# Kernel optimization log

Hardware: AMD Instinct MI355X
Metric: run time of the kernel (lower is better)

Reference implementation:

```python
import jax, jax.numpy as jnp
import numpy as np

REGION = (4, 4, 4)
NHEAD = 4
HEAD_DIM = 64
SCALE = HEAD_DIM ** -0.5
NUM_MODALITIES = 4


def _grid2seq(x, region, nhead):
    # x: [B, C, H, W, D] -> [B, nhead, n_regions, region_cube, head_dim]
    B, C, H, W, D = x.shape
    rh, rw, rd = H // region[0], W // region[1], D // region[2]
    hd = C // nhead
    x = x.reshape(B, nhead, hd, rh, region[0], rw, region[1], rd, region[2])
    x = x.transpose(0, 1, 3, 5, 7, 4, 6, 8, 2)  # bmchpwqdr -> bmhwdpqrc
    return x.reshape(B, nhead, rh * rw * rd, region[0] * region[1] * region[2], hd), rh, rw, rd


def _seq2grid(x, rh, rw, rd, region):
    # x: [B, nhead, n_regions, region_cube, head_dim] -> [B, C, H, W, D]
    B, nhead, nreg, rc, hd = x.shape
    x = x.reshape(B, nhead, rh, rw, rd, region[0], region[1], region[2], hd)
    x = x.transpose(0, 1, 8, 2, 5, 3, 6, 4, 7)  # bmhwdpqrc -> bmchpwqdr
    return x.reshape(B, nhead * hd, rh * region[0], rw * region[1], rd * region[2])


def _gather_regions(kv_seq, rg):
    # kv_seq: [B, H, kvN, kc, hd], rg: [B, H, qN, topk] -> [B, H, qN, topk, kc, hd]
    return jax.vmap(jax.vmap(lambda k, g: k[g]))(kv_seq, rg)


def setup_inputs() -> dict:
    key = jax.random.key(0)
    ks = jax.random.split(key, 20)
    shp = (2, 256, 16, 16, 16)
    inp = {"mask": jnp.ones((2, 4), dtype=jnp.int32)}
    names = [f"{p}{i}" for p in ("q", "k", "v") for i in range(4)]
    for n, kk in zip(names, ks[:12]):
        inp[n] = jax.random.normal(kk, shp, dtype=jnp.float32)
    for i, kk in zip(range(4), ks[12:16]):
        inp[f"rg{i}"] = jax.random.randint(kk, (2, 4, 64, 4), 0, 64, dtype=jnp.int32)
    return inp


def reference(mask, q0, q1, q2, q3, k0, k1, k2, k3, v0, v1, v2, v3, rg0, rg1, rg2, rg3):
    qs = [q0, q1, q2, q3]
    ks = [k0, k1, k2, k3]
    vs = [v0, v1, v2, v3]
    rgs = [rg0, rg1, rg2, rg3]

    q_seq, rh, rw, rd = zip(*[(g[0], g[1], g[2], g[3]) for g in [_grid2seq(q, REGION, NHEAD) for q in qs]])
    rh, rw, rd = rh[0], rw[0], rd[0]

    key_parts, val_parts = [], []
    for k_, v_, rg_ in zip(ks, vs, rgs):
        kseq, _, _, _ = _grid2seq(k_, REGION, NHEAD)
        vseq, _, _, _ = _grid2seq(v_, REGION, NHEAD)
        B, H, kvN, kc, hd = kseq.shape
        qN = rg_.shape[2]
        kg = _gather_regions(kseq, rg_).reshape(B, H, qN, -1, hd)  # [B,H,qN,topk*kc,hd]
        vg = _gather_regions(vseq, rg_).reshape(B, H, qN, -1, hd)
        key_parts.append(kg)
        val_parts.append(vg)
    key_g = jnp.concatenate(key_parts, axis=-2)  # [B,H,qN, M*topk*kc, hd]
    value_g = jnp.concatenate(val_parts, axis=-2)

    N = key_g.shape[-2]
    rep = N // NUM_MODALITIES
    mask_full = jnp.repeat(mask[:, None, None, None, :], rep, axis=-1)  # [B,1,1,1,N]

    outs = []
    for q in q_seq:
        attn = jnp.einsum("bhnqc,bhnkc->bhnqk", q * SCALE, key_g)
        attn = jnp.where(mask_full == 0, -jnp.inf, attn)
        attn = jax.nn.softmax(attn, axis=-1)
        o = jnp.einsum("bhnqk,bhnkc->bhnqc", attn, value_g)
        outs.append(_seq2grid(o, rh, rw, rd, REGION))
    return jnp.stack(outs, axis=0)  # [M, B, C, H, W, D]
```

## Files before the change

kernel.cpp:

```cpp
#include <hip/hip_runtime.h>
#include <hip/hip_bf16.h>

typedef short v8s __attribute__((ext_vector_type(8)));
typedef float v4f __attribute__((ext_vector_type(4)));

#define LDK 72
#define SCALE_LOG2E 0.18033688f
#define RESCALE_THR 8.0f

struct MMRAParams {
    const float* q[4];
    const float* k[4];
    const float* v[4];
    const int*   rg[4];
    const int*   mask;
    float*       out;
};

__device__ __forceinline__ unsigned pkbf(float a, float b) {
    unsigned r;
    asm("v_cvt_pk_bf16_f32 %0, %1, %2" : "=v"(r) : "v"(a), "v"(b));
    return r;
}

__global__ __launch_bounds__(256, 2)
void mmra_attn(MMRAParams P) {
    const int bid = blockIdx.x;
    const int h = bid & 3;
    const int b = (bid >> 2) & 1;
    const int n = bid >> 3;
    const int H0 = ((n >> 4) & 3) << 2;
    const int W0 = ((n >> 2) & 3) << 2;
    const int D0 = (n & 3) << 2;

    const int tid  = threadIdx.x;
    const int wave = tid >> 6;
    const int lane = tid & 63;
    const int l15  = lane & 15;
    const int quad = lane >> 4;

    __shared__ __align__(16) ushort Klds[64 * LDK];
    __shared__ __align__(16) ushort Vlds[64 * LDK];
    __shared__ __align__(16) ushort Plds[4][64 * LDK];

    const int bh_base = (b * 256 + h * 64) * 4096;
    const int rgbase  = ((b * 4 + h) * 64 + n) * 4;

    const bool actm[4] = { P.mask[b * 4 + 0] != 0, P.mask[b * 4 + 1] != 0,
                           P.mask[b * 4 + 2] != 0, P.mask[b * 4 + 3] != 0 };

    auto kptr = [&](int m) { return (m == 0) ? P.k[0] : (m == 1) ? P.k[1] : (m == 2) ? P.k[2] : P.k[3]; };
    auto vptr = [&](int m) { return (m == 0) ? P.v[0] : (m == 1) ? P.v[1] : (m == 2) ? P.v[2] : P.v[3]; };
    auto rptr = [&](int m) { return (m == 0) ? P.rg[0] : (m == 1) ? P.rg[1] : (m == 2) ? P.rg[2] : P.rg[3]; };

    float4 pkf[4], pvf[4];
    auto prefetch = [&](int cj) {
        const int mod = cj >> 2, j = cj & 3;
        const int g = rptr(mod)[rgbase + j] & 63;
        const int goff = (((g >> 4) & 3) << 10) + (((g >> 2) & 3) << 6) + ((g & 3) << 2);
        const float* ks = kptr(mod);
        const float* vs = vptr(mod);
        const int off0 = bh_base + lane * 4096 + goff;
        #pragma unroll
        for (int i = 0; i < 4; ++i) {
            const int pq = wave * 4 + i;
            const int off = off0 + (pq >> 2) * 256 + (pq & 3) * 16;
            pkf[i] = *(const float4*)(ks + off);
            pvf[i] = *(const float4*)(vs + off);
        }
    };

    prefetch(0);

    v8s qfrag[4][2];
    {
        ushort* qbuf = &Plds[wave][0];
        const float* qsrc = (wave == 0) ? P.q[0] : (wave == 1) ? P.q[1] : (wave == 2) ? P.q[2] : P.q[3];
        #pragma unroll
        for (int rb = 0; rb < 4; ++rb) {
            #pragma unroll
            for (int i = 0; i < 4; ++i) {
                int off = bh_base + lane * 4096 + (H0 + rb) * 256 + (W0 + i) * 16 + D0;
                float4 cv = *(const float4*)(qsrc + off);
                unsigned q01 = pkbf(cv.x * SCALE_LOG2E, cv.y * SCALE_LOG2E);
                unsigned q23 = pkbf(cv.z * SCALE_LOG2E, cv.w * SCALE_LOG2E);
                ushort* qb = &qbuf[(rb * 16 + i * 4) * LDK + lane];
                qb[0 * LDK] = (ushort)q01;
                qb[1 * LDK] = (ushort)(q01 >> 16);
                qb[2 * LDK] = (ushort)q23;
                qb[3 * LDK] = (ushort)(q23 >> 16);
            }
        }
        __asm__ volatile("s_waitcnt lgkmcnt(0)" ::: "memory");
        #pragma unroll
        for (int rb = 0; rb < 4; ++rb) {
            qfrag[rb][0] = *(const v8s*)&qbuf[(rb * 16 + l15) * LDK + quad * 8];
            qfrag[rb][1] = *(const v8s*)&qbuf[(rb * 16 + l15) * LDK + 32 + quad * 8];
        }
    }

    v4f  oacc[4][4];
    float mrow[4], lrow[4];
    #pragma unroll
    for (int mt = 0; mt < 4; ++mt) {
        mrow[mt] = -1e30f; lrow[mt] = 0.f;
        #pragma unroll
        for (int nt = 0; nt < 4; ++nt) oacc[mt][nt] = (v4f){0.f, 0.f, 0.f, 0.f};
    }

    #pragma unroll 1
    for (int cj = 0; cj < 16; ++cj) {
        const bool act = actm[cj >> 2];
        if (act) {
            __syncthreads();
            #pragma unroll
            for (int i = 0; i < 4; ++i) {
                const int pq = wave * 4 + i;
                unsigned k01 = pkbf(pkf[i].x, pkf[i].y);
                unsigned k23 = pkbf(pkf[i].z, pkf[i].w);
                ushort* kb = &Klds[(pq * 4) * LDK + lane];
                kb[0 * LDK] = (ushort)k01;
                kb[1 * LDK] = (ushort)(k01 >> 16);
                kb[2 * LDK] = (ushort)k23;
                kb[3 * LDK] = (ushort)(k23 >> 16);
                uint2 vv;
                vv.x = pkbf(pvf[i].x, pvf[i].y);
                vv.y = pkbf(pvf[i].z, pvf[i].w);
                *(uint2*)&Vlds[lane * LDK + pq * 4] = vv;
            }
        }
        if (cj < 15) prefetch(cj + 1);
        if (!act) continue;
        __syncthreads();

        {
            v8s kfrag[4][2];
            #pragma unroll
            for (int t = 0; t < 4; ++t) {
                kfrag[t][0] = *(const v8s*)&Klds[(t * 16 + l15) * LDK + quad * 8];
                kfrag[t][1] = *(const v8s*)&Klds[(t * 16 + l15) * LDK + 32 + quad * 8];
            }
            #pragma unroll
            for (int mt = 0; mt < 4; ++mt) {
                float sv[4][4];
                #pragma unroll
                for (int nt = 0; nt < 4; ++nt) {
                    v4f acc = (v4f){0.f, 0.f, 0.f, 0.f};
                    acc = __builtin_amdgcn_mfma_f32_16x16x32_bf16(kfrag[nt][0], qfrag[mt][0], acc, 0, 0, 0);
                    acc = __builtin_amdgcn_mfma_f32_16x16x32_bf16(kfrag[nt][1], qfrag[mt][1], acc, 0, 0, 0);
                    #pragma unroll
                    for (int r = 0; r < 4; ++r) sv[nt][r] = acc[r];
                }
                float mx;
                {
                    float a0 = fmaxf(fmaxf(sv[0][0], sv[0][1]), sv[0][2]);
                    float a1 = fmaxf(fmaxf(sv[0][3], sv[1][0]), sv[1][1]);
                    float a2 = fmaxf(fmaxf(sv[1][2], sv[1][3]), sv[2][0]);
                    float a3 = fmaxf(fmaxf(sv[2][1], sv[2][2]), sv[2][3]);
                    float a4 = fmaxf(fmaxf(sv[3][0], sv[3][1]), sv[3][2]);
                    mx = fmaxf(fmaxf(fmaxf(a0, a1), a2), fmaxf(fmaxf(a3, a4), sv[3][3]));
                }
                mx = fmaxf(mx, __shfl_xor(mx, 16));
                mx = fmaxf(mx, __shfl_xor(mx, 32));

                if (!__all(mx - mrow[mt] <= RESCALE_THR)) {
                    const float mnew  = fmaxf(mrow[mt], mx);
                    const float alpha = exp2f(mrow[mt] - mnew);
                    mrow[mt] = mnew;
                    lrow[mt] *= alpha;
                    float alpha_row[4];
                    #pragma unroll
                    for (int r = 0; r < 4; ++r)
                        alpha_row[r] = __shfl(alpha, (quad << 4) | (quad * 4 + r));
                    #pragma unroll
                    for (int nt = 0; nt < 4; ++nt)
                        #pragma unroll
                        for (int r = 0; r < 4; ++r) oacc[mt][nt][r] *= alpha_row[r];
                }
                const float mcur = mrow[mt];

                float rsum = 0.f;
                #pragma unroll
                for (int nt = 0; nt < 4; ++nt) {
                    float p0 = exp2f(sv[nt][0] - mcur);
                    float p1 = exp2f(sv[nt][1] - mcur);
                    float p2 = exp2f(sv[nt][2] - mcur);
                    float p3 = exp2f(sv[nt][3] - mcur);
                    rsum += (p0 + p1) + (p2 + p3);
                    uint2 pw;
                    pw.x = pkbf(p0, p1);
                    pw.y = pkbf(p2, p3);
                    *(uint2*)&Plds[wave][(mt * 16 + l15) * LDK + nt * 16 + quad * 4] = pw;
                }
                rsum += __shfl_xor(rsum, 16);
                rsum += __shfl_xor(rsum, 32);
                lrow[mt] += rsum;
            }
        }

        __asm__ volatile("s_waitcnt lgkmcnt(0)" ::: "memory");
        {
            v8s vfrag[4][2];
            #pragma unroll
            for (int t = 0; t < 4; ++t) {
                vfrag[t][0] = *(const v8s*)&Vlds[(t * 16 + l15) * LDK + quad * 8];
                vfrag[t][1] = *(const v8s*)&Vlds[(t * 16 + l15) * LDK + 32 + quad * 8];
            }
            #pragma unroll
            for (int mt = 0; mt < 4; ++mt) {
                v8s pf0 = *(const v8s*)&Plds[wave][(mt * 16 + l15) * LDK + quad * 8];
                v8s pf1 = *(const v8s*)&Plds[wave][(mt * 16 + l15) * LDK + 32 + quad * 8];
                #pragma unroll
                for (int nt = 0; nt < 4; ++nt) {
                    oacc[mt][nt] = __builtin_amdgcn_mfma_f32_16x16x32_bf16(pf0, vfrag[nt][0], oacc[mt][nt], 0, 0, 0);
                    oacc[mt][nt] = __builtin_amdgcn_mfma_f32_16x16x32_bf16(pf1, vfrag[nt][1], oacc[mt][nt], 0, 0, 0);
                }
            }
        }
    }

    const int obase = (wave * 2 + b) * 1048576 + h * 64 * 4096;
    #pragma unroll
    for (int mt = 0; mt < 4; ++mt) {
        const float invq = 1.0f / lrow[mt];
        float inv_row[4];
        #pragma unroll
        for (int r = 0; r < 4; ++r)
            inv_row[r] = __shfl(invq, (quad << 4) | (quad * 4 + r));
        #pragma unroll
        for (int nt = 0; nt < 4; ++nt) {
            float4 ov;
            ov.x = oacc[mt][nt][0] * inv_row[0];
            ov.y = oacc[mt][nt][1] * inv_row[1];
            ov.z = oacc[mt][nt][2] * inv_row[2];
            ov.w = oacc[mt][nt][3] * inv_row[3];
            int off = obase + (nt * 16 + l15) * 4096 + (H0 + mt) * 256 + (W0 + quad) * 16 + D0;
            *(float4*)(P.out + off) = ov;
        }
    }
}

extern "C" void kernel_launch(void* const* d_in, const int* in_sizes, int n_in,
                              void* d_out, int out_size, void* d_ws, size_t ws_size,
                              hipStream_t stream) {
    (void)in_sizes; (void)n_in; (void)out_size; (void)d_ws; (void)ws_size;
    MMRAParams P;
    P.mask = (const int*)d_in[0];
    for (int i = 0; i < 4; ++i) {
        P.q[i]  = (const float*)d_in[1 + i];
        P.k[i]  = (const float*)d_in[5 + i];
        P.v[i]  = (const float*)d_in[9 + i];
        P.rg[i] = (const int*)d_in[13 + i];
    }
    P.out = (float*)d_out;
    hipLaunchKernelGGL(mmra_attn, dim3(512), dim3(256), 0, stream, P);
}
```

Before: 238.5 us.

## Split query rows across 8 waves and keep P in registers for PV

Doubles the block to 512 threads so each of the 8 waves handles half of one modality's query rows. K and V staging work per wave is halved. The P matrix is no longer written to and read back from LDS: its register layout is fed directly into 16x16x16 bf16 MFMAs against transposed V fragments, removing the per-wave P buffers and a wait on LDS. It relies on the accumulator layout matching the MFMA A-operand layout, and it doubles the MFMA instruction count for PV because each instruction covers half the K depth.

```diff
diff --git a/kernel.cpp b/kernel.cpp
--- a/kernel.cpp
+++ b/kernel.cpp
@@ -2,6 +2,7 @@
 #include <hip/hip_bf16.h>
 
 typedef short v8s __attribute__((ext_vector_type(8)));
+typedef short v4s __attribute__((ext_vector_type(4)));
 typedef float v4f __attribute__((ext_vector_type(4)));
 
 #define LDK 72
@@ -23,7 +24,18 @@
     return r;
 }
 
-__global__ __launch_bounds__(256, 2)
+__device__ __forceinline__ v4f mfma16(v4s a, v4s b, v4f c) {
+#if __has_builtin(__builtin_amdgcn_mfma_f32_16x16x16bf16_1k)
+    return __builtin_amdgcn_mfma_f32_16x16x16bf16_1k(a, b, c, 0, 0, 0);
+#elif __has_builtin(__builtin_amdgcn_mfma_f32_16x16x16_bf16)
+    return __builtin_amdgcn_mfma_f32_16x16x16_bf16(a, b, c, 0, 0, 0);
+#else
+    asm("v_mfma_f32_16x16x16_bf16 %0, %1, %2, %0" : "+v"(c) : "v"(a), "v"(b));
+    return c;
+#endif
+}
+
+__global__ __launch_bounds__(512, 4)
 void mmra_attn(MMRAParams P) {
     const int bid = blockIdx.x;
     const int h = bid & 3;
@@ -35,13 +47,15 @@
 
     const int tid  = threadIdx.x;
     const int wave = tid >> 6;
+    const int qm   = wave >> 1;
+    const int mth  = wave & 1;
     const int lane = tid & 63;
     const int l15  = lane & 15;
     const int quad = lane >> 4;
 
-    __shared__ __align__(16) ushort Klds[64 * LDK];
-    __shared__ __align__(16) ushort Vlds[64 * LDK];
-    __shared__ __align__(16) ushort Plds[4][64 * LDK];
+    __shared__ __align__(16) ushort SMEM[18432];
+    ushort* Klds = SMEM;
+    ushort* Vlds = SMEM + 4608;
 
     const int bh_base = (b * 256 + h * 64) * 4096;
     const int rgbase  = ((b * 4 + h) * 64 + n) * 4;
@@ -53,7 +67,7 @@
     auto vptr = [&](int m) { return (m == 0) ? P.v[0] : (m == 1) ? P.v[1] : (m == 2) ? P.v[2] : P.v[3]; };
     auto rptr = [&](int m) { return (m == 0) ? P.rg[0] : (m == 1) ? P.rg[1] : (m == 2) ? P.rg[2] : P.rg[3]; };
 
-    float4 pkf[4], pvf[4];
+    float4 pkf[2], pvf[2];
     auto prefetch = [&](int cj) {
         const int mod = cj >> 2, j = cj & 3;
         const int g = rptr(mod)[rgbase + j] & 63;
@@ -62,8 +76,8 @@
         const float* vs = vptr(mod);
         const int off0 = bh_base + lane * 4096 + goff;
         #pragma unroll
-        for (int i = 0; i < 4; ++i) {
-            const int pq = wave * 4 + i;
+        for (int i = 0; i < 2; ++i) {
+            const int pq = wave * 2 + i;
             const int off = off0 + (pq >> 2) * 256 + (pq & 3) * 16;
             pkf[i] = *(const float4*)(ks + off);
             pvf[i] = *(const float4*)(vs + off);
@@ -72,19 +86,20 @@
 
     prefetch(0);
 
-    v8s qfrag[4][2];
+    v8s qfrag[2][2];
     {
-        ushort* qbuf = &Plds[wave][0];
-        const float* qsrc = (wave == 0) ? P.q[0] : (wave == 1) ? P.q[1] : (wave == 2) ? P.q[2] : P.q[3];
-        #pragma unroll
-        for (int rb = 0; rb < 4; ++rb) {
+        ushort* qbuf = SMEM + wave * 2304;
+        const float* qsrc = (qm == 0) ? P.q[0] : (qm == 1) ? P.q[1] : (qm == 2) ? P.q[2] : P.q[3];
+        #pragma unroll
+        for (int rb2 = 0; rb2 < 2; ++rb2) {
+            const int rb = mth * 2 + rb2;
             #pragma unroll
             for (int i = 0; i < 4; ++i) {
                 int off = bh_base + lane * 4096 + (H0 + rb) * 256 + (W0 + i) * 16 + D0;
                 float4 cv = *(const float4*)(qsrc + off);
                 unsigned q01 = pkbf(cv.x * SCALE_LOG2E, cv.y * SCALE_LOG2E);
                 unsigned q23 = pkbf(cv.z * SCALE_LOG2E, cv.w * SCALE_LOG2E);
-                ushort* qb = &qbuf[(rb * 16 + i * 4) * LDK + lane];
+                ushort* qb = &qbuf[(rb2 * 16 + i * 4) * LDK + lane];
                 qb[0 * LDK] = (ushort)q01;
                 qb[1 * LDK] = (ushort)(q01 >> 16);
                 qb[2 * LDK] = (ushort)q23;
@@ -93,19 +108,19 @@
         }
         __asm__ volatile("s_waitcnt lgkmcnt(0)" ::: "memory");
         #pragma unroll
-        for (int rb = 0; rb < 4; ++rb) {
-            qfrag[rb][0] = *(const v8s*)&qbuf[(rb * 16 + l15) * LDK + quad * 8];
-            qfrag[rb][1] = *(const v8s*)&qbuf[(rb * 16 + l15) * LDK + 32 + quad * 8];
-        }
-    }
-
-    v4f  oacc[4][4];
-    float mrow[4], lrow[4];
+        for (int m2 = 0; m2 < 2; ++m2) {
+            qfrag[m2][0] = *(const v8s*)&qbuf[(m2 * 16 + l15) * LDK + quad * 8];
+            qfrag[m2][1] = *(const v8s*)&qbuf[(m2 * 16 + l15) * LDK + 32 + quad * 8];
+        }
+    }
+
+    v4f  oacc[2][4];
+    float mrow[2], lrow[2];
     #pragma unroll
-    for (int mt = 0; mt < 4; ++mt) {
-        mrow[mt] = -1e30f; lrow[mt] = 0.f;
-        #pragma unroll
-        for (int nt = 0; nt < 4; ++nt) oacc[mt][nt] = (v4f){0.f, 0.f, 0.f, 0.f};
+    for (int m2 = 0; m2 < 2; ++m2) {
+        mrow[m2] = -1e30f; lrow[m2] = 0.f;
+        #pragma unroll
+        for (int t = 0; t < 4; ++t) oacc[m2][t] = (v4f){0.f, 0.f, 0.f, 0.f};
     }
 
     #pragma unroll 1
@@ -114,8 +129,8 @@
         if (act) {
             __syncthreads();
             #pragma unroll
-            for (int i = 0; i < 4; ++i) {
-                const int pq = wave * 4 + i;
+            for (int i = 0; i < 2; ++i) {
+                const int pq = wave * 2 + i;
                 unsigned k01 = pkbf(pkf[i].x, pkf[i].y);
                 unsigned k23 = pkbf(pkf[i].z, pkf[i].w);
                 ushort* kb = &Klds[(pq * 4) * LDK + lane];
@@ -133,108 +148,97 @@
         if (!act) continue;
         __syncthreads();
 
+        uint2 pa[2][4];
         {
-            v8s kfrag[4][2];
-            #pragma unroll
-            for (int t = 0; t < 4; ++t) {
-                kfrag[t][0] = *(const v8s*)&Klds[(t * 16 + l15) * LDK + quad * 8];
-                kfrag[t][1] = *(const v8s*)&Klds[(t * 16 + l15) * LDK + 32 + quad * 8];
-            }
-            #pragma unroll
-            for (int mt = 0; mt < 4; ++mt) {
-                float sv[4][4];
+            float sv[2][4][4];
+            #pragma unroll
+            for (int nt = 0; nt < 4; ++nt) {
+                v8s kf0 = *(const v8s*)&Klds[(nt * 16 + l15) * LDK + quad * 8];
+                v8s kf1 = *(const v8s*)&Klds[(nt * 16 + l15) * LDK + 32 + quad * 8];
                 #pragma unroll
-                for (int nt = 0; nt < 4; ++nt) {
+                for (int m2 = 0; m2 < 2; ++m2) {
                     v4f acc = (v4f){0.f, 0.f, 0.f, 0.f};
-                    acc = __builtin_amdgcn_mfma_f32_16x16x32_bf16(kfrag[nt][0], qfrag[mt][0], acc, 0, 0, 0);
-                    acc = __builtin_amdgcn_mfma_f32_16x16x32_bf16(kfrag[nt][1], qfrag[mt][1], acc, 0, 0, 0);
+                    acc = __builtin_amdgcn_mfma_f32_16x16x32_bf16(kf0, qfrag[m2][0], acc, 0, 0, 0);
+                    acc = __builtin_amdgcn_mfma_f32_16x16x32_bf16(kf1, qfrag[m2][1], acc, 0, 0, 0);
                     #pragma unroll
-                    for (int r = 0; r < 4; ++r) sv[nt][r] = acc[r];
-                }
+                    for (int r = 0; r < 4; ++r) sv[m2][nt][r] = acc[r];
+                }
+            }
+            #pragma unroll
+            for (int m2 = 0; m2 < 2; ++m2) {
                 float mx;
                 {
-                    float a0 = fmaxf(fmaxf(sv[0][0], sv[0][1]), sv[0][2]);
-                    float a1 = fmaxf(fmaxf(sv[0][3], sv[1][0]), sv[1][1]);
-                    float a2 = fmaxf(fmaxf(sv[1][2], sv[1][3]), sv[2][0]);
-                    float a3 = fmaxf(fmaxf(sv[2][1], sv[2][2]), sv[2][3]);
-                    float a4 = fmaxf(fmaxf(sv[3][0], sv[3][1]), sv[3][2]);
-                    mx = fmaxf(fmaxf(fmaxf(a0, a1), a2), fmaxf(fmaxf(a3, a4), sv[3][3]));
+                    float a0 = fmaxf(fmaxf(sv[m2][0][0], sv[m2][0][1]), sv[m2][0][2]);
+                    float a1 = fmaxf(fmaxf(sv[m2][0][3], sv[m2][1][0]), sv[m2][1][1]);
+                    float a2 = fmaxf(fmaxf(sv[m2][1][2], sv[m2][1][3]), sv[m2][2][0]);
+                    float a3 = fmaxf(fmaxf(sv[m2][2][1], sv[m2][2][2]), sv[m2][2][3]);
+                    float a4 = fmaxf(fmaxf(sv[m2][3][0], sv[m2][3][1]), sv[m2][3][2]);
+                    mx = fmaxf(fmaxf(fmaxf(a0, a1), a2), fmaxf(fmaxf(a3, a4), sv[m2][3][3]));
                 }
                 mx = fmaxf(mx, __shfl_xor(mx, 16));
                 mx = fmaxf(mx, __shfl_xor(mx, 32));
 
-                if (!__all(mx - mrow[mt] <= RESCALE_THR)) {
-                    const float mnew  = fmaxf(mrow[mt], mx);
-                    const float alpha = exp2f(mrow[mt] - mnew);
-                    mrow[mt] = mnew;
-                    lrow[mt] *= alpha;
+                if (!__all(mx - mrow[m2] <= RESCALE_THR)) {
+                    const float mnew  = fmaxf(mrow[m2], mx);
+                    const float alpha = exp2f(mrow[m2] - mnew);
+                    mrow[m2] = mnew;
+                    lrow[m2] *= alpha;
                     float alpha_row[4];
                     #pragma unroll
                     for (int r = 0; r < 4; ++r)
                         alpha_row[r] = __shfl(alpha, (quad << 4) | (quad * 4 + r));
                     #pragma unroll
-                    for (int nt = 0; nt < 4; ++nt)
+                    for (int t = 0; t < 4; ++t)
                         #pragma unroll
-                        for (int r = 0; r < 4; ++r) oacc[mt][nt][r] *= alpha_row[r];
-                }
-                const float mcur = mrow[mt];
+                        for (int r = 0; r < 4; ++r) oacc[m2][t][r] *= alpha_row[r];
+                }
+                const float mcur = mrow[m2];
 
                 float rsum = 0.f;
                 #pragma unroll
                 for (int nt = 0; nt < 4; ++nt) {
-                    float p0 = exp2f(sv[nt][0] - mcur);
-                    float p1 = exp2f(sv[nt][1] - mcur);
-                    float p2 = exp2f(sv[nt][2] - mcur);
-                    float p3 = exp2f(sv[nt][3] - mcur);
+                    float p0 = exp2f(sv[m2][nt][0] - mcur);
+                    float p1 = exp2f(sv[m2][nt][1] - mcur);
+                    float p2 = exp2f(sv[m2][nt][2] - mcur);
+                    float p3 = exp2f(sv[m2][nt][3] - mcur);
                     rsum += (p0 + p1) + (p2 + p3);
-                    uint2 pw;
-                    pw.x = pkbf(p0, p1);
-                    pw.y = pkbf(p2, p3);
-                    *(uint2*)&Plds[wave][(mt * 16 + l15) * LDK + nt * 16 + quad * 4] = pw;
+                    pa[m2][nt].x = pkbf(p0, p1);
+                    pa[m2][nt].y = pkbf(p2, p3);
                 }
                 rsum += __shfl_xor(rsum, 16);
                 rsum += __shfl_xor(rsum, 32);
-                lrow[mt] += rsum;
-            }
-        }
-
-        __asm__ volatile("s_waitcnt lgkmcnt(0)" ::: "memory");
-        {
-            v8s vfrag[4][2];
-            #pragma unroll
-            for (int t = 0; t < 4; ++t) {
-                vfrag[t][0] = *(const v8s*)&Vlds[(t * 16 + l15) * LDK + quad * 8];
-                vfrag[t][1] = *(const v8s*)&Vlds[(t * 16 + l15) * LDK + 32 + quad * 8];
-            }
-            #pragma unroll
-            for (int mt = 0; mt < 4; ++mt) {
-                v8s pf0 = *(const v8s*)&Plds[wave][(mt * 16 + l15) * LDK + quad * 8];
-                v8s pf1 = *(const v8s*)&Plds[wave][(mt * 16 + l15) * LDK + 32 + quad * 8];
-                #pragma unroll
-                for (int nt = 0; nt < 4; ++nt) {
-                    oacc[mt][nt] = __builtin_amdgcn_mfma_f32_16x16x32_bf16(pf0, vfrag[nt][0], oacc[mt][nt], 0, 0, 0);
-                    oacc[mt][nt] = __builtin_amdgcn_mfma_f32_16x16x32_bf16(pf1, vfrag[nt][1], oacc[mt][nt], 0, 0, 0);
-                }
-            }
-        }
-    }
-
-    const int obase = (wave * 2 + b) * 1048576 + h * 64 * 4096;
+                lrow[m2] += rsum;
+            }
+        }
+
+        #pragma unroll
+        for (int t = 0; t < 4; ++t) {
+            #pragma unroll
+            for (int nt = 0; nt < 4; ++nt) {
+                v4s vf = *(const v4s*)&Vlds[(t * 16 + l15) * LDK + nt * 16 + quad * 4];
+                oacc[0][t] = mfma16(__builtin_bit_cast(v4s, pa[0][nt]), vf, oacc[0][t]);
+                oacc[1][t] = mfma16(__builtin_bit_cast(v4s, pa[1][nt]), vf, oacc[1][t]);
+            }
+        }
+    }
+
+    const int obase = (qm * 2 + b) * 1048576 + h * 64 * 4096;
     #pragma unroll
-    for (int mt = 0; mt < 4; ++mt) {
-        const float invq = 1.0f / lrow[mt];
+    for (int m2 = 0; m2 < 2; ++m2) {
+        const int mt = mth * 2 + m2;
+        const float invq = 1.0f / lrow[m2];
         float inv_row[4];
         #pragma unroll
         for (int r = 0; r < 4; ++r)
             inv_row[r] = __shfl(invq, (quad << 4) | (quad * 4 + r));
         #pragma unroll
-        for (int nt = 0; nt < 4; ++nt) {
+        for (int t = 0; t < 4; ++t) {
             float4 ov;
-            ov.x = oacc[mt][nt][0] * inv_row[0];
-            ov.y = oacc[mt][nt][1] * inv_row[1];
-            ov.z = oacc[mt][nt][2] * inv_row[2];
-            ov.w = oacc[mt][nt][3] * inv_row[3];
-            int off = obase + (nt * 16 + l15) * 4096 + (H0 + mt) * 256 + (W0 + quad) * 16 + D0;
+            ov.x = oacc[m2][t][0] * inv_row[0];
+            ov.y = oacc[m2][t][1] * inv_row[1];
+            ov.z = oacc[m2][t][2] * inv_row[2];
+            ov.w = oacc[m2][t][3] * inv_row[3];
+            int off = obase + (t * 16 + l15) * 4096 + (H0 + mt) * 256 + (W0 + quad) * 16 + D0;
             *(float4*)(P.out + off) = ov;
         }
     }
@@ -253,5 +257,5 @@
         P.rg[i] = (const int*)d_in[13 + i];
     }
     P.out = (float*)d_out;
-    hipLaunchKernelGGL(mmra_attn, dim3(512), dim3(256), 0, stream, P);
-}
+    hipLaunchKernelGGL(mmra_attn, dim3(512), dim3(512), 0, stream, P);
+}
```

Measured after the change: 240.4 us. Within noise of the previous version (+0.8%).

## Double-buffer K/V in LDS and keep P in registers for PV MFMA

Applied to the files above, without the earlier changes.

Replaces the single K/V LDS buffer with a double buffer, so the next chunk is staged while the current one is computed, and drops one barrier per iteration. It precomputes a list of active modality chunks so masked chunks are skipped without per-iteration branching. The softmax probabilities stay in registers and feed 16x16x16 bf16 MFMAs directly instead of going through a per-wave P buffer in LDS. It also adds s_setprio around the MFMA blocks. The cost is more live registers (the full score tile plus packed P), which could reduce occupancy or cause spills, and twice as many smaller MFMAs in the PV product.

```diff
diff --git a/kernel.cpp b/kernel.cpp
--- a/kernel.cpp
+++ b/kernel.cpp
@@ -2,6 +2,7 @@
 #include <hip/hip_bf16.h>
 
 typedef short v8s __attribute__((ext_vector_type(8)));
+typedef short v4s __attribute__((ext_vector_type(4)));
 typedef float v4f __attribute__((ext_vector_type(4)));
 
 #define LDK 72
@@ -21,6 +22,17 @@
     unsigned r;
     asm("v_cvt_pk_bf16_f32 %0, %1, %2" : "=v"(r) : "v"(a), "v"(b));
     return r;
+}
+
+__device__ __forceinline__ v4f mfma16(v4s a, v4s b, v4f c) {
+#if __has_builtin(__builtin_amdgcn_mfma_f32_16x16x16bf16_1k)
+    return __builtin_amdgcn_mfma_f32_16x16x16bf16_1k(a, b, c, 0, 0, 0);
+#elif __has_builtin(__builtin_amdgcn_mfma_f32_16x16x16_bf16)
+    return __builtin_amdgcn_mfma_f32_16x16x16_bf16(a, b, c, 0, 0, 0);
+#else
+    asm("v_mfma_f32_16x16x16_bf16 %0, %1, %2, %0" : "+v"(c) : "v"(a), "v"(b));
+    return c;
+#endif
 }
 
 __global__ __launch_bounds__(256, 2)
@@ -39,9 +51,7 @@
     const int l15  = lane & 15;
     const int quad = lane >> 4;
 
-    __shared__ __align__(16) ushort Klds[64 * LDK];
-    __shared__ __align__(16) ushort Vlds[64 * LDK];
-    __shared__ __align__(16) ushort Plds[4][64 * LDK];
+    __shared__ __align__(16) ushort SMEM[18432];
 
     const int bh_base = (b * 256 + h * 64) * 4096;
     const int rgbase  = ((b * 4 + h) * 64 + n) * 4;
@@ -52,6 +62,14 @@
     auto kptr = [&](int m) { return (m == 0) ? P.k[0] : (m == 1) ? P.k[1] : (m == 2) ? P.k[2] : P.k[3]; };
     auto vptr = [&](int m) { return (m == 0) ? P.v[0] : (m == 1) ? P.v[1] : (m == 2) ? P.v[2] : P.v[3]; };
     auto rptr = [&](int m) { return (m == 0) ? P.rg[0] : (m == 1) ? P.rg[1] : (m == 2) ? P.rg[2] : P.rg[3]; };
+
+    unsigned long long clist = 0ull; int nc = 0;
+    for (int m = 0; m < 4; ++m) {
+        if (actm[m]) {
+            #pragma unroll
+            for (int s = 0; s < 4; ++s) { clist |= ((unsigned long long)(m * 4 + s)) << (4 * nc); ++nc; }
+        }
+    }
 
     float4 pkf[4], pvf[4];
     auto prefetch = [&](int cj) {
@@ -70,11 +88,31 @@
         }
     };
 
-    prefetch(0);
+    auto stage = [&](int buf) {
+        ushort* Kb = SMEM + buf * 9216;
+        ushort* Vb = Kb + 4608;
+        #pragma unroll
+        for (int i = 0; i < 4; ++i) {
+            const int pq = wave * 4 + i;
+            unsigned k01 = pkbf(pkf[i].x, pkf[i].y);
+            unsigned k23 = pkbf(pkf[i].z, pkf[i].w);
+            ushort* kb = &Kb[(pq * 4) * LDK + lane];
+            kb[0 * LDK] = (ushort)k01;
+            kb[1 * LDK] = (ushort)(k01 >> 16);
+            kb[2 * LDK] = (ushort)k23;
+            kb[3 * LDK] = (ushort)(k23 >> 16);
+            uint2 vv;
+            vv.x = pkbf(pvf[i].x, pvf[i].y);
+            vv.y = pkbf(pvf[i].z, pvf[i].w);
+            *(uint2*)&Vb[lane * LDK + pq * 4] = vv;
+        }
+    };
+
+    prefetch((int)(clist & 15));
 
     v8s qfrag[4][2];
     {
-        ushort* qbuf = &Plds[wave][0];
+        ushort* qbuf = SMEM + wave * 4608;
         const float* qsrc = (wave == 0) ? P.q[0] : (wave == 1) ? P.q[1] : (wave == 2) ? P.q[2] : P.q[3];
         #pragma unroll
         for (int rb = 0; rb < 4; ++rb) {
@@ -98,6 +136,10 @@
             qfrag[rb][1] = *(const v8s*)&qbuf[(rb * 16 + l15) * LDK + 32 + quad * 8];
         }
     }
+    __syncthreads();
+    stage(0);
+    if (nc > 1) prefetch((int)((clist >> 4) & 15));
+    __syncthreads();
 
     v4f  oacc[4][4];
     float mrow[4], lrow[4];
@@ -105,118 +147,97 @@
     for (int mt = 0; mt < 4; ++mt) {
         mrow[mt] = -1e30f; lrow[mt] = 0.f;
         #pragma unroll
-        for (int nt = 0; nt < 4; ++nt) oacc[mt][nt] = (v4f){0.f, 0.f, 0.f, 0.f};
-    }
-
+        for (int t = 0; t < 4; ++t) oacc[mt][t] = (v4f){0.f, 0.f, 0.f, 0.f};
+    }
+
+    int cur = 0;
     #pragma unroll 1
-    for (int cj = 0; cj < 16; ++cj) {
-        const bool act = actm[cj >> 2];
-        if (act) {
-            __syncthreads();
-            #pragma unroll
-            for (int i = 0; i < 4; ++i) {
-                const int pq = wave * 4 + i;
-                unsigned k01 = pkbf(pkf[i].x, pkf[i].y);
-                unsigned k23 = pkbf(pkf[i].z, pkf[i].w);
-                ushort* kb = &Klds[(pq * 4) * LDK + lane];
-                kb[0 * LDK] = (ushort)k01;
-                kb[1 * LDK] = (ushort)(k01 >> 16);
-                kb[2 * LDK] = (ushort)k23;
-                kb[3 * LDK] = (ushort)(k23 >> 16);
-                uint2 vv;
-                vv.x = pkbf(pvf[i].x, pvf[i].y);
-                vv.y = pkbf(pvf[i].z, pvf[i].w);
-                *(uint2*)&Vlds[lane * LDK + pq * 4] = vv;
-            }
-        }
-        if (cj < 15) prefetch(cj + 1);
-        if (!act) continue;
+    for (int i = 0; i < nc; ++i) {
+        if (i + 1 < nc) {
+            stage(cur ^ 1);
+            if (i + 2 < nc) prefetch((int)((clist >> (4 * (i + 2))) & 15));
+        }
+        const ushort* Kb = SMEM + cur * 9216;
+        const ushort* Vb = Kb + 4608;
+
+        float sv[4][4][4];
+        #pragma unroll
+        for (int nt = 0; nt < 4; ++nt) {
+            v8s kf0 = *(const v8s*)&Kb[(nt * 16 + l15) * LDK + quad * 8];
+            v8s kf1 = *(const v8s*)&Kb[(nt * 16 + l15) * LDK + 32 + quad * 8];
+            __builtin_amdgcn_s_setprio(1);
+            #pragma unroll
+            for (int mt = 0; mt < 4; ++mt) {
+                v4f acc = (v4f){0.f, 0.f, 0.f, 0.f};
+                acc = __builtin_amdgcn_mfma_f32_16x16x32_bf16(kf0, qfrag[mt][0], acc, 0, 0, 0);
+                acc = __builtin_amdgcn_mfma_f32_16x16x32_bf16(kf1, qfrag[mt][1], acc, 0, 0, 0);
+                #pragma unroll
+                for (int r = 0; r < 4; ++r) sv[mt][nt][r] = acc[r];
+            }
+            __builtin_amdgcn_s_setprio(0);
+        }
+        uint2 pa[4][4];
+        #pragma unroll
+        for (int mt = 0; mt < 4; ++mt) {
+            float mx;
+            {
+                float a0 = fmaxf(fmaxf(sv[mt][0][0], sv[mt][0][1]), sv[mt][0][2]);
+                float a1 = fmaxf(fmaxf(sv[mt][0][3], sv[mt][1][0]), sv[mt][1][1]);
+                float a2 = fmaxf(fmaxf(sv[mt][1][2], sv[mt][1][3]), sv[mt][2][0]);
+                float a3 = fmaxf(fmaxf(sv[mt][2][1], sv[mt][2][2]), sv[mt][2][3]);
+                float a4 = fmaxf(fmaxf(sv[mt][3][0], sv[mt][3][1]), sv[mt][3][2]);
+                mx = fmaxf(fmaxf(fmaxf(a0, a1), a2), fmaxf(fmaxf(a3, a4), sv[mt][3][3]));
+            }
+            mx = fmaxf(mx, __shfl_xor(mx, 16));
+            mx = fmaxf(mx, __shfl_xor(mx, 32));
+
+            if (!__all(mx - mrow[mt] <= RESCALE_THR)) {
+                const float mnew  = fmaxf(mrow[mt], mx);
+                const float alpha = exp2f(mrow[mt] - mnew);
+                mrow[mt] = mnew;
+                lrow[mt] *= alpha;
+                float alpha_row[4];
+                #pragma unroll
+                for (int r = 0; r < 4; ++r)
+                    alpha_row[r] = __shfl(alpha, (quad << 4) | (quad * 4 + r));
+                #pragma unroll
+                for (int t = 0; t < 4; ++t)
+                    #pragma unroll
+                    for (int r = 0; r < 4; ++r) oacc[mt][t][r] *= alpha_row[r];
+            }
+            const float mcur = mrow[mt];
+
+            float rsum = 0.f;
+            #pragma unroll
+            for (int nt = 0; nt < 4; ++nt) {
+                float p0 = exp2f(sv[mt][nt][0] - mcur);
+                float p1 = exp2f(sv[mt][nt][1] - mcur);
+                float p2 = exp2f(sv[mt][nt][2] - mcur);
+                float p3 = exp2f(sv[mt][nt][3] - mcur);
+                rsum += (p0 + p1) + (p2 + p3);
+                pa[mt][nt].x = pkbf(p0, p1);
+                pa[mt][nt].y = pkbf(p2, p3);
+            }
+            rsum += __shfl_xor(rsum, 16);
+            rsum += __shfl_xor(rsum, 32);
+            lrow[mt] += rsum;
+        }
+
+        __builtin_amdgcn_s_setprio(1);
+        #pragma unroll
+        for (int t = 0; t < 4; ++t) {
+            #pragma unroll
+            for (int nt = 0; nt < 4; ++nt) {
+                v4s vf = *(const v4s*)&Vb[(t * 16 + l15) * LDK + nt * 16 + quad * 4];
+                #pragma unroll
+                for (int mt = 0; mt < 4; ++mt)
+                    oacc[mt][t] = mfma16(__builtin_bit_cast(v4s, pa[mt][nt]), vf, oacc[mt][t]);
+            }
+        }
+        __builtin_amdgcn_s_setprio(0);
+
         __syncthreads();
-
-        {
-            v8s kfrag[4][2];
-            #pragma unroll
-            for (int t = 0; t < 4; ++t) {
-                kfrag[t][0] = *(const v8s*)&Klds[(t * 16 + l15) * LDK + quad * 8];
-                kfrag[t][1] = *(const v8s*)&Klds[(t * 16 + l15) * LDK + 32 + quad * 8];
-            }
-            #pragma unroll
-            for (int mt = 0; mt < 4; ++mt) {
-                float sv[4][4];
-                #pragma unroll
-                for (int nt = 0; nt < 4; ++nt) {
-                    v4f acc = (v4f){0.f, 0.f, 0.f, 0.f};
-                    acc = __builtin_amdgcn_mfma_f32_16x16x32_bf16(kfrag[nt][0], qfrag[mt][0], acc, 0, 0, 0);
-                    acc = __builtin_amdgcn_mfma_f32_16x16x32_bf16(kfrag[nt][1], qfrag[mt][1], acc, 0, 0, 0);
-                    #pragma unroll
-                    for (int r = 0; r < 4; ++r) sv[nt][r] = acc[r];
-                }
-                float mx;
-                {
-                    float a0 = fmaxf(fmaxf(sv[0][0], sv[0][1]), sv[0][2]);
-                    float a1 = fmaxf(fmaxf(sv[0][3], sv[1][0]), sv[1][1]);
-                    float a2 = fmaxf(fmaxf(sv[1][2], sv[1][3]), sv[2][0]);
-                    float a3 = fmaxf(fmaxf(sv[2][1], sv[2][2]), sv[2][3]);
-                    float a4 = fmaxf(fmaxf(sv[3][0], sv[3][1]), sv[3][2]);
-                    mx = fmaxf(fmaxf(fmaxf(a0, a1), a2), fmaxf(fmaxf(a3, a4), sv[3][3]));
-                }
-                mx = fmaxf(mx, __shfl_xor(mx, 16));
-                mx = fmaxf(mx, __shfl_xor(mx, 32));
-
-                if (!__all(mx - mrow[mt] <= RESCALE_THR)) {
-                    const float mnew  = fmaxf(mrow[mt], mx);
-                    const float alpha = exp2f(mrow[mt] - mnew);
-                    mrow[mt] = mnew;
-                    lrow[mt] *= alpha;
-                    float alpha_row[4];
-                    #pragma unroll
-                    for (int r = 0; r < 4; ++r)
-                        alpha_row[r] = __shfl(alpha, (quad << 4) | (quad * 4 + r));
-                    #pragma unroll
-                    for (int nt = 0; nt < 4; ++nt)
-                        #pragma unroll
-                        for (int r = 0; r < 4; ++r) oacc[mt][nt][r] *= alpha_row[r];
-                }
-                const float mcur = mrow[mt];
-
-                float rsum = 0.f;
-                #pragma unroll
-                for (int nt = 0; nt < 4; ++nt) {
-                    float p0 = exp2f(sv[nt][0] - mcur);
-                    float p1 = exp2f(sv[nt][1] - mcur);
-                    float p2 = exp2f(sv[nt][2] - mcur);
-                    float p3 = exp2f(sv[nt][3] - mcur);
-                    rsum += (p0 + p1) + (p2 + p3);
-                    uint2 pw;
-                    pw.x = pkbf(p0, p1);
-                    pw.y = pkbf(p2, p3);
-                    *(uint2*)&Plds[wave][(mt * 16 + l15) * LDK + nt * 16 + quad * 4] = pw;
-                }
-                rsum += __shfl_xor(rsum, 16);
-                rsum += __shfl_xor(rsum, 32);
-                lrow[mt] += rsum;
-            }
-        }
-
-        __asm__ volatile("s_waitcnt lgkmcnt(0)" ::: "memory");
-        {
-            v8s vfrag[4][2];
-            #pragma unroll
-            for (int t = 0; t < 4; ++t) {
-                vfrag[t][0] = *(const v8s*)&Vlds[(t * 16 + l15) * LDK + quad * 8];
-                vfrag[t][1] = *(const v8s*)&Vlds[(t * 16 + l15) * LDK + 32 + quad * 8];
-            }
-            #pragma unroll
-            for (int mt = 0; mt < 4; ++mt) {
-                v8s pf0 = *(const v8s*)&Plds[wave][(mt * 16 + l15) * LDK + quad * 8];
-                v8s pf1 = *(const v8s*)&Plds[wave][(mt * 16 + l15) * LDK + 32 + quad * 8];
-                #pragma unroll
-                for (int nt = 0; nt < 4; ++nt) {
-                    oacc[mt][nt] = __builtin_amdgcn_mfma_f32_16x16x32_bf16(pf0, vfrag[nt][0], oacc[mt][nt], 0, 0, 0);
-                    oacc[mt][nt] = __builtin_amdgcn_mfma_f32_16x16x32_bf16(pf1, vfrag[nt][1], oacc[mt][nt], 0, 0, 0);
-                }
-            }
-        }
+        cur ^= 1;
     }
 
     const int obase = (wave * 2 + b) * 1048576 + h * 64 * 4096;
@@ -228,13 +249,13 @@
         for (int r = 0; r < 4; ++r)
             inv_row[r] = __shfl(invq, (quad << 4) | (quad * 4 + r));
         #pragma unroll
-        for (int nt = 0; nt < 4; ++nt) {
+        for (int t = 0; t < 4; ++t) {
             float4 ov;
-            ov.x = oacc[mt][nt][0] * inv_row[0];
-            ov.y = oacc[mt][nt][1] * inv_row[1];
-            ov.z = oacc[mt][nt][2] * inv_row[2];
-            ov.w = oacc[mt][nt][3] * inv_row[3];
-            int off = obase + (nt * 16 + l15) * 4096 + (H0 + mt) * 256 + (W0 + quad) * 16 + D0;
+            ov.x = oacc[mt][t][0] * inv_row[0];
+            ov.y = oacc[mt][t][1] * inv_row[1];
+            ov.z = oacc[mt][t][2] * inv_row[2];
+            ov.w = oacc[mt][t][3] * inv_row[3];
+            int off = obase + (t * 16 + l15) * 4096 + (H0 + mt) * 256 + (W0 + quad) * 16 + D0;
             *(float4*)(P.out + off) = ov;
         }
     }
```

Result: no change. 240.4 us (+0.8%).
